# Optimization experiments

Measured on AMD Instinct MI355X. Metric: run time of the kernel, lower is better.

Reference implementation:

```python
import jax, jax.numpy as jnp
import numpy as np
from math import comb

DEGREE = 3


def build_index_tables(n, degree):
    """For each degree d in [2, degree], build (first, rest) int arrays so that
    row_d = x[first] * row_{d-1}[rest], where row_d lists the values of all
    ordered (multiset) degree-d monomials in lexicographic order.
    An ordered d-tuple starting with i has its tail t[1:] being an ordered
    (d-1)-tuple with elements in [i, n); in lexicographic order these occupy
    the tail of row_{d-1}, starting at prev_len - comb(n-i+d-2, d-1)."""
    tables = []
    prev_len = n  # row_1 = x itself
    for d in range(2, degree + 1):
        starts = np.array([prev_len - comb(n - i + d - 2, d - 1) for i in range(n)], dtype=np.int64)
        rest = np.concatenate([np.arange(s, prev_len, dtype=np.int32) for s in starts])
        first = np.repeat(np.arange(n, dtype=np.int32), prev_len - starts)
        tables.append((jnp.asarray(first), jnp.asarray(rest)))
        prev_len = rest.shape[0]
    return tables


def setup_inputs() -> dict:
    key = jax.random.key(0)
    n, out_size = 256, 32
    ks = jax.random.split(key, 5)
    sizes = [comb(n + d - 1, d) for d in range(DEGREE + 1)]  # [1, 256, 32896, 2829056]
    inp = {"x": jax.random.normal(ks[0], (n,), dtype=jnp.float32)}
    for d in range(DEGREE + 1):
        fan_in = sizes[d]
        bound = 1.0 / np.sqrt(fan_in)  # kaiming_uniform with a=sqrt(5)
        inp[f"coeff_deg_{d}"] = jax.random.uniform(
            ks[d + 1], (out_size, fan_in), dtype=jnp.float32, minval=-bound, maxval=bound)
    return inp


def reference(x, coeff_deg_0, coeff_deg_1, coeff_deg_2, coeff_deg_3):
    n = x.shape[0]
    tables = build_index_tables(n, DEGREE)  # static numpy work at trace time
    rows = [jnp.ones((1,), dtype=x.dtype), x]
    for first, rest in tables:
        rows.append(x[first] * rows[-1][rest])  # gather + elementwise product
    coeffs = [coeff_deg_0, coeff_deg_1, coeff_deg_2, coeff_deg_3]
    out = coeffs[0] @ rows[0]
    for c, r in zip(coeffs[1:], rows[1:]):
        out = out + c @ r  # (out_size, m_d) @ (m_d,) -> (out_size,)
    return out
```

## Files before the change

### kernel.cpp

```cpp
#include <hip/hip_runtime.h>

constexpr int N   = 256;
constexpr int OUT = 32;
constexpr int OPG = 8;
constexpr int OG  = OUT / OPG;
constexpr int M2  = 32896;
constexpr int M3  = 2829056;
constexpr int Q3  = M3 / 4;
constexpr int Q2  = M2 / 4;
constexpr int BX  = 256;
constexpr int IT3 = 11;
constexpr int D2_FIRST = 208;

typedef float f32x4 __attribute__((ext_vector_type(4)));

__device__ __forceinline__ int c3_tail(int s) {
    return s * (s + 1) * (s + 2) / 6;
}

__global__ __launch_bounds__(256, 4) void poly_partial(
    const float* __restrict__ x, const float* __restrict__ c2,
    const float* __restrict__ c3, float* __restrict__ partial)
{
    __shared__ float xs[N];
    const int tid = threadIdx.x;
    if (tid < N) xs[tid] = x[tid];
    __syncthreads();

    const int bx = blockIdx.x;
    const int g  = blockIdx.y;

    float acc[OPG];
#pragma unroll
    for (int oo = 0; oo < OPG; ++oo) acc[oo] = 0.f;

    const float* __restrict__ c3g = c3 + (size_t)g * OPG * M3;

    for (int it = 0; it < IT3; ++it) {
        const int q = bx * 256 + tid + it * (BX * 256);
        if (q < Q3) {
            const int base = q * 4;
            int lo = 0, hi = N - 1;
            while (lo < hi) {
                int mid = (lo + hi + 1) >> 1;
                int O = M3 - c3_tail(N - mid);
                if (O <= base) lo = mid; else hi = mid - 1;
            }
            const int i = lo;
            const int s = N - i;
            const int rem = base - (M3 - c3_tail(s));
            lo = 0; hi = s - 1;
            while (lo < hi) {
                int mid = (lo + hi + 1) >> 1;
                int A = mid * s - (mid * (mid - 1)) / 2;
                if (A <= rem) lo = mid; else hi = mid - 1;
            }
            const int a = lo;
            int ii = i, j = i + a, k = j + (rem - (a * s - (a * (a - 1)) / 2));

            float v[4];
#pragma unroll
            for (int t = 0; t < 4; ++t) {
                v[t] = xs[ii] * xs[j] * xs[k];
                ++k;
                if (k == N) { ++j; if (j == N) { ++ii; j = ii; } k = j; }
            }
            const float* p = c3g + base;
#pragma unroll
            for (int oo = 0; oo < OPG; ++oo) {
                const f32x4 c = __builtin_nontemporal_load(
                    reinterpret_cast<const f32x4*>(p + (size_t)oo * M3));
                acc[oo] += c[0] * v[0] + c[1] * v[1] + c[2] * v[2] + c[3] * v[3];
            }
        }
    }

    if (bx >= D2_FIRST) {
        const int q = (bx - D2_FIRST) * 256 + tid;
        if (q < Q2) {
            const int base = q * 4;
            int lo = 0, hi = N - 1;
            while (lo < hi) {
                int mid = (lo + hi + 1) >> 1;
                int O = mid * N - (mid * (mid - 1)) / 2;
                if (O <= base) lo = mid; else hi = mid - 1;
            }
            int j = lo;
            int k = j + (base - (j * N - (j * (j - 1)) / 2));
            float v[4];
#pragma unroll
            for (int t = 0; t < 4; ++t) {
                v[t] = xs[j] * xs[k];
                ++k;
                if (k == N) { ++j; k = j; }
            }
            const float* p = c2 + (size_t)g * OPG * M2 + base;
#pragma unroll
            for (int oo = 0; oo < OPG; ++oo) {
                const f32x4 c = __builtin_nontemporal_load(
                    reinterpret_cast<const f32x4*>(p + (size_t)oo * M2));
                acc[oo] += c[0] * v[0] + c[1] * v[1] + c[2] * v[2] + c[3] * v[3];
            }
        }
    }

    __shared__ float red[4][OPG];
    const int lane = tid & 63, wid = tid >> 6;
#pragma unroll
    for (int oo = 0; oo < OPG; ++oo) {
        float a = acc[oo];
#pragma unroll
        for (int off = 32; off > 0; off >>= 1) a += __shfl_down(a, off);
        if (lane == 0) red[wid][oo] = a;
    }
    __syncthreads();
    if (tid < OPG) {
        partial[((size_t)g * BX + bx) * OPG + tid] =
            red[0][tid] + red[1][tid] + red[2][tid] + red[3][tid];
    }
}

__global__ __launch_bounds__(1024) void poly_final(
    const float* __restrict__ partial, const float* __restrict__ x,
    const float* __restrict__ c0, const float* __restrict__ c1,
    float* __restrict__ out)
{
    __shared__ float lds[1024];
    const int tid = threadIdx.x;
    const int o = tid & 31, c = tid >> 5;
    const int g = o >> 3, oo = o & 7;

    float a = 0.f;
#pragma unroll
    for (int r = 0; r < BX / 32; ++r) {
        const int b = c + r * 32;
        a += partial[((size_t)g * BX + b) * OPG + oo];
    }
#pragma unroll
    for (int e = 0; e < 8; ++e) {
        const int k = c * 8 + e;
        a += c1[o * N + k] * x[k];
    }
    if (c == 0) a += c0[o];
    lds[tid] = a;
    __syncthreads();
    if (tid < 32) {
        float s = 0.f;
#pragma unroll
        for (int cc = 0; cc < 32; ++cc) s += lds[cc * 32 + tid];
        out[tid] = s;
    }
}

extern "C" void kernel_launch(void* const* d_in, const int* in_sizes, int n_in,
                              void* d_out, int out_size, void* d_ws, size_t ws_size,
                              hipStream_t stream) {
    const float* x  = (const float*)d_in[0];
    const float* c0 = (const float*)d_in[1];
    const float* c1 = (const float*)d_in[2];
    const float* c2 = (const float*)d_in[3];
    const float* c3 = (const float*)d_in[4];
    float* out     = (float*)d_out;
    float* partial = (float*)d_ws;

    dim3 grid(BX, OG);
    poly_partial<<<grid, 256, 0, stream>>>(x, c2, c3, partial);
    poly_final<<<1, 1024, 0, stream>>>(partial, x, c0, c1, out);
}
```

Measured before the change: 69.41 us.

## Process eight monomials per thread with contiguous per-block ranges and parallel final reduce

Each thread now handles 8 consecutive degree-3 (and degree-2) monomials, loading two float4 vectors per output row. The index binary searches are amortised over twice as many elements. Work is split into contiguous balanced chunks per block instead of a strided interleave, and degree-2 work is spread across all blocks. The final kernel runs 32 blocks that reduce with wave shuffles instead of a single 1024-thread block. Memory traffic per block becomes a contiguous range, which may change DRAM access locality; per-thread register use rises.

```diff
diff --git a/kernel.cpp b/kernel.cpp
--- a/kernel.cpp
+++ b/kernel.cpp
@@ -6,11 +6,14 @@
 constexpr int OG  = OUT / OPG;
 constexpr int M2  = 32896;
 constexpr int M3  = 2829056;
-constexpr int Q3  = M3 / 4;
-constexpr int Q2  = M2 / 4;
+constexpr int P3  = M3 / 8;
+constexpr int P2  = M2 / 8;
 constexpr int BX  = 256;
-constexpr int IT3 = 11;
-constexpr int D2_FIRST = 208;
+constexpr int K3  = P3 / BX;
+constexpr int R3  = P3 % BX;
+constexpr int K2  = P2 / BX;
+constexpr int R2  = P2 % BX;
+constexpr int IT3 = (K3 + 1 + 255) / 256;
 
 typedef float f32x4 __attribute__((ext_vector_type(4)));
 
@@ -34,51 +37,59 @@
 #pragma unroll
     for (int oo = 0; oo < OPG; ++oo) acc[oo] = 0.f;
 
-    const float* __restrict__ c3g = c3 + (size_t)g * OPG * M3;
+    {
+        const int s3 = bx * K3 + (bx < R3 ? bx : R3);
+        const int n3 = K3 + (bx < R3 ? 1 : 0);
+        const float* __restrict__ c3g = c3 + (size_t)g * OPG * M3;
+        for (int it = 0; it < IT3; ++it) {
+            const int r = it * 256 + tid;
+            if (r < n3) {
+                const int base = (s3 + r) * 8;
+                int lo = 0, hi = N - 1;
+                while (lo < hi) {
+                    int mid = (lo + hi + 1) >> 1;
+                    int O = M3 - c3_tail(N - mid);
+                    if (O <= base) lo = mid; else hi = mid - 1;
+                }
+                const int i = lo;
+                const int s = N - i;
+                const int rem = base - (M3 - c3_tail(s));
+                lo = 0; hi = s - 1;
+                while (lo < hi) {
+                    int mid = (lo + hi + 1) >> 1;
+                    int A = mid * s - (mid * (mid - 1)) / 2;
+                    if (A <= rem) lo = mid; else hi = mid - 1;
+                }
+                const int a = lo;
+                int ii = i, j = i + a, k = j + (rem - (a * s - (a * (a - 1)) / 2));
 
-    for (int it = 0; it < IT3; ++it) {
-        const int q = bx * 256 + tid + it * (BX * 256);
-        if (q < Q3) {
-            const int base = q * 4;
-            int lo = 0, hi = N - 1;
-            while (lo < hi) {
-                int mid = (lo + hi + 1) >> 1;
-                int O = M3 - c3_tail(N - mid);
-                if (O <= base) lo = mid; else hi = mid - 1;
-            }
-            const int i = lo;
-            const int s = N - i;
-            const int rem = base - (M3 - c3_tail(s));
-            lo = 0; hi = s - 1;
-            while (lo < hi) {
-                int mid = (lo + hi + 1) >> 1;
-                int A = mid * s - (mid * (mid - 1)) / 2;
-                if (A <= rem) lo = mid; else hi = mid - 1;
-            }
-            const int a = lo;
-            int ii = i, j = i + a, k = j + (rem - (a * s - (a * (a - 1)) / 2));
-
-            float v[4];
+                float v[8];
 #pragma unroll
-            for (int t = 0; t < 4; ++t) {
-                v[t] = xs[ii] * xs[j] * xs[k];
-                ++k;
-                if (k == N) { ++j; if (j == N) { ++ii; j = ii; } k = j; }
-            }
-            const float* p = c3g + base;
+                for (int t = 0; t < 8; ++t) {
+                    v[t] = xs[ii] * xs[j] * xs[k];
+                    ++k;
+                    if (k == N) { ++j; if (j == N) { ++ii; j = ii; } k = j; }
+                }
+                const float* p = c3g + (size_t)base;
 #pragma unroll
-            for (int oo = 0; oo < OPG; ++oo) {
-                const f32x4 c = __builtin_nontemporal_load(
-                    reinterpret_cast<const f32x4*>(p + (size_t)oo * M3));
-                acc[oo] += c[0] * v[0] + c[1] * v[1] + c[2] * v[2] + c[3] * v[3];
+                for (int oo = 0; oo < OPG; ++oo) {
+                    const float* sp = p + (size_t)oo * M3;
+                    const f32x4 ca = __builtin_nontemporal_load(
+                        reinterpret_cast<const f32x4*>(sp));
+                    const f32x4 cb = __builtin_nontemporal_load(
+                        reinterpret_cast<const f32x4*>(sp + 4));
+                    acc[oo] += ca[0] * v[0] + ca[1] * v[1] + ca[2] * v[2] + ca[3] * v[3]
+                             + cb[0] * v[4] + cb[1] * v[5] + cb[2] * v[6] + cb[3] * v[7];
+                }
             }
         }
     }
 
-    if (bx >= D2_FIRST) {
-        const int q = (bx - D2_FIRST) * 256 + tid;
-        if (q < Q2) {
-            const int base = q * 4;
+    {
+        const int s2 = bx * K2 + (bx < R2 ? bx : R2);
+        const int n2 = K2 + (bx < R2 ? 1 : 0);
+        if (tid < n2) {
+            const int base = (s2 + tid) * 8;
             int lo = 0, hi = N - 1;
             while (lo < hi) {
                 int mid = (lo + hi + 1) >> 1;
@@ -87,9 +98,9 @@
             }
             int j = lo;
             int k = j + (base - (j * N - (j * (j - 1)) / 2));
-            float v[4];
+            float v[8];
 #pragma unroll
-            for (int t = 0; t < 4; ++t) {
+            for (int t = 0; t < 8; ++t) {
                 v[t] = xs[j] * xs[k];
                 ++k;
                 if (k == N) { ++j; k = j; }
@@ -97,9 +108,13 @@
             const float* p = c2 + (size_t)g * OPG * M2 + base;
 #pragma unroll
             for (int oo = 0; oo < OPG; ++oo) {
-                const f32x4 c = __builtin_nontemporal_load(
-                    reinterpret_cast<const f32x4*>(p + (size_t)oo * M2));
-                acc[oo] += c[0] * v[0] + c[1] * v[1] + c[2] * v[2] + c[3] * v[3];
+                const float* sp = p + (size_t)oo * M2;
+                const f32x4 ca = __builtin_nontemporal_load(
+                    reinterpret_cast<const f32x4*>(sp));
+                const f32x4 cb = __builtin_nontemporal_load(
+                    reinterpret_cast<const f32x4*>(sp + 4));
+                acc[oo] += ca[0] * v[0] + ca[1] * v[1] + ca[2] * v[2] + ca[3] * v[3]
+                         + cb[0] * v[4] + cb[1] * v[5] + cb[2] * v[6] + cb[3] * v[7];
             }
         }
     }
@@ -120,36 +135,26 @@
     }
 }
 
-__global__ __launch_bounds__(1024) void poly_final(
+__global__ __launch_bounds__(256) void poly_final(
     const float* __restrict__ partial, const float* __restrict__ x,
     const float* __restrict__ c0, const float* __restrict__ c1,
     float* __restrict__ out)
 {
-    __shared__ float lds[1024];
+    const int o = blockIdx.x;
+    const int g = o >> 3, oo = o & 7;
     const int tid = threadIdx.x;
-    const int o = tid & 31, c = tid >> 5;
-    const int g = o >> 3, oo = o & 7;
 
-    float a = 0.f;
+    float a = partial[((size_t)g * BX + tid) * OPG + oo]
+            + c1[o * N + tid] * x[tid];
+
+    __shared__ float red[4];
+    const int lane = tid & 63, wid = tid >> 6;
 #pragma unroll
-    for (int r = 0; r < BX / 32; ++r) {
-        const int b = c + r * 32;
-        a += partial[((size_t)g * BX + b) * OPG + oo];
-    }
-#pragma unroll
-    for (int e = 0; e < 8; ++e) {
-        const int k = c * 8 + e;
-        a += c1[o * N + k] * x[k];
-    }
-    if (c == 0) a += c0[o];
-    lds[tid] = a;
+    for (int off = 32; off > 0; off >>= 1) a += __shfl_down(a, off);
+    if (lane == 0) red[wid] = a;
     __syncthreads();
-    if (tid < 32) {
-        float s = 0.f;
-#pragma unroll
-        for (int cc = 0; cc < 32; ++cc) s += lds[cc * 32 + tid];
-        out[tid] = s;
-    }
+    if (tid == 0)
+        out[o] = red[0] + red[1] + red[2] + red[3] + c0[o];
 }
 
 extern "C" void kernel_launch(void* const* d_in, const int* in_sizes, int n_in,
@@ -165,5 +170,5 @@
 
     dim3 grid(BX, OG);
     poly_partial<<<grid, 256, 0, stream>>>(x, c2, c3, partial);
-    poly_final<<<1, 1024, 0, stream>>>(partial, x, c0, c1, out);
+    poly_final<<<OUT, 256, 0, stream>>>(partial, x, c0, c1, out);
 }
```

After: 87.99 us. +26.8%, slower.

## Double-buffer degree-3 coefficient loads and parallelize final reduction across blocks

Applied to the files above, without the earlier changes.

The degree-3 loop is unrolled into templated steps that issue the next iteration's eight 16-byte coefficient loads into a second register buffer before computing the current monomials, so memory latency overlaps with the index binary searches. The monomial computation also hoists the x[i]*x[j] product. The final kernel now uses 32 blocks of 256 threads with wave shuffles instead of one 1024-thread block. The extra prefetch buffers raise register pressure, which could hurt occupancy under launch_bounds(256,4).

```diff
diff --git a/kernel.cpp b/kernel.cpp
--- a/kernel.cpp
+++ b/kernel.cpp
@@ -18,6 +18,61 @@
     return s * (s + 1) * (s + 2) / 6;
 }
 
+template<int IT>
+__device__ __forceinline__ void step3(const float* __restrict__ c3g,
+                                      const float* xs, int q0,
+                                      f32x4 (&cons)[OPG], f32x4 (&pref)[OPG],
+                                      float (&acc)[OPG])
+{
+    if constexpr (IT + 1 < IT3) {
+        const int qn = q0 + (IT + 1) * (BX * 256);
+        if (qn < Q3) {
+            const float* pn = c3g + (size_t)qn * 4;
+#pragma unroll
+            for (int oo = 0; oo < OPG; ++oo)
+                pref[oo] = __builtin_nontemporal_load(
+                    reinterpret_cast<const f32x4*>(pn + (size_t)oo * M3));
+        }
+    }
+    const int q = q0 + IT * (BX * 256);
+    if (q < Q3) {
+        const int base = q * 4;
+        int lo = 0, hi = N - 1;
+        while (lo < hi) {
+            int mid = (lo + hi + 1) >> 1;
+            int O = M3 - c3_tail(N - mid);
+            if (O <= base) lo = mid; else hi = mid - 1;
+        }
+        const int i0 = lo;
+        const int s = N - i0;
+        const int rem = base - (M3 - c3_tail(s));
+        lo = 0; hi = s - 1;
+        while (lo < hi) {
+            int mid = (lo + hi + 1) >> 1;
+            int A = mid * s - (mid * (mid - 1)) / 2;
+            if (A <= rem) lo = mid; else hi = mid - 1;
+        }
+        const int a = lo;
+        int ii = i0, j = i0 + a, k = j + (rem - (a * s - (a * (a - 1)) / 2));
+
+        float pre = xs[ii] * xs[j];
+        float v[4];
+#pragma unroll
+        for (int t = 0; t < 4; ++t) {
+            v[t] = pre * xs[k];
+            ++k;
+            if (k == N) {
+                ++j; if (j == N) { ++ii; j = ii; }
+                k = j; pre = xs[ii] * xs[j];
+            }
+        }
+#pragma unroll
+        for (int oo = 0; oo < OPG; ++oo)
+            acc[oo] += cons[oo][0] * v[0] + cons[oo][1] * v[1]
+                     + cons[oo][2] * v[2] + cons[oo][3] * v[3];
+    }
+}
+
 __global__ __launch_bounds__(256, 4) void poly_partial(
     const float* __restrict__ x, const float* __restrict__ c2,
     const float* __restrict__ c3, float* __restrict__ partial)
@@ -31,54 +86,40 @@
     const int g  = blockIdx.y;
 
     float acc[OPG];
-#pragma unroll
-    for (int oo = 0; oo < OPG; ++oo) acc[oo] = 0.f;
+    f32x4 bufA[OPG], bufB[OPG];
+#pragma unroll
+    for (int oo = 0; oo < OPG; ++oo) {
+        acc[oo] = 0.f;
+        bufA[oo] = f32x4{0.f, 0.f, 0.f, 0.f};
+        bufB[oo] = f32x4{0.f, 0.f, 0.f, 0.f};
+    }
 
     const float* __restrict__ c3g = c3 + (size_t)g * OPG * M3;
-
-    for (int it = 0; it < IT3; ++it) {
-        const int q = bx * 256 + tid + it * (BX * 256);
-        if (q < Q3) {
-            const int base = q * 4;
-            int lo = 0, hi = N - 1;
-            while (lo < hi) {
-                int mid = (lo + hi + 1) >> 1;
-                int O = M3 - c3_tail(N - mid);
-                if (O <= base) lo = mid; else hi = mid - 1;
-            }
-            const int i = lo;
-            const int s = N - i;
-            const int rem = base - (M3 - c3_tail(s));
-            lo = 0; hi = s - 1;
-            while (lo < hi) {
-                int mid = (lo + hi + 1) >> 1;
-                int A = mid * s - (mid * (mid - 1)) / 2;
-                if (A <= rem) lo = mid; else hi = mid - 1;
-            }
-            const int a = lo;
-            int ii = i, j = i + a, k = j + (rem - (a * s - (a * (a - 1)) / 2));
-
-            float v[4];
-#pragma unroll
-            for (int t = 0; t < 4; ++t) {
-                v[t] = xs[ii] * xs[j] * xs[k];
-                ++k;
-                if (k == N) { ++j; if (j == N) { ++ii; j = ii; } k = j; }
-            }
-            const float* p = c3g + base;
-#pragma unroll
-            for (int oo = 0; oo < OPG; ++oo) {
-                const f32x4 c = __builtin_nontemporal_load(
-                    reinterpret_cast<const f32x4*>(p + (size_t)oo * M3));
-                acc[oo] += c[0] * v[0] + c[1] * v[1] + c[2] * v[2] + c[3] * v[3];
-            }
-        }
-    }
+    const int q0 = bx * 256 + tid;
+
+    {
+        const float* p0 = c3g + (size_t)q0 * 4;
+#pragma unroll
+        for (int oo = 0; oo < OPG; ++oo)
+            bufA[oo] = __builtin_nontemporal_load(
+                reinterpret_cast<const f32x4*>(p0 + (size_t)oo * M3));
+    }
+    step3<0>(c3g, xs, q0, bufA, bufB, acc);
+    step3<1>(c3g, xs, q0, bufB, bufA, acc);
+    step3<2>(c3g, xs, q0, bufA, bufB, acc);
+    step3<3>(c3g, xs, q0, bufB, bufA, acc);
+    step3<4>(c3g, xs, q0, bufA, bufB, acc);
+    step3<5>(c3g, xs, q0, bufB, bufA, acc);
+    step3<6>(c3g, xs, q0, bufA, bufB, acc);
+    step3<7>(c3g, xs, q0, bufB, bufA, acc);
+    step3<8>(c3g, xs, q0, bufA, bufB, acc);
+    step3<9>(c3g, xs, q0, bufB, bufA, acc);
+    step3<10>(c3g, xs, q0, bufA, bufB, acc);
 
     if (bx >= D2_FIRST) {
-        const int q = (bx - D2_FIRST) * 256 + tid;
-        if (q < Q2) {
-            const int base = q * 4;
+        const int qq = (bx - D2_FIRST) * 256 + tid;
+        if (qq < Q2) {
+            const int base = qq * 4;
             int lo = 0, hi = N - 1;
             while (lo < hi) {
                 int mid = (lo + hi + 1) >> 1;
@@ -87,12 +128,13 @@
             }
             int j = lo;
             int k = j + (base - (j * N - (j * (j - 1)) / 2));
+            float pre = xs[j];
             float v[4];
 #pragma unroll
             for (int t = 0; t < 4; ++t) {
-                v[t] = xs[j] * xs[k];
+                v[t] = pre * xs[k];
                 ++k;
-                if (k == N) { ++j; k = j; }
+                if (k == N) { ++j; k = j; pre = xs[j]; }
             }
             const float* p = c2 + (size_t)g * OPG * M2 + base;
 #pragma unroll
@@ -120,36 +162,26 @@
     }
 }
 
-__global__ __launch_bounds__(1024) void poly_final(
+__global__ __launch_bounds__(256) void poly_final(
     const float* __restrict__ partial, const float* __restrict__ x,
     const float* __restrict__ c0, const float* __restrict__ c1,
     float* __restrict__ out)
 {
-    __shared__ float lds[1024];
+    const int o = blockIdx.x;
+    const int g = o >> 3, oo = o & 7;
     const int tid = threadIdx.x;
-    const int o = tid & 31, c = tid >> 5;
-    const int g = o >> 3, oo = o & 7;
-
-    float a = 0.f;
-#pragma unroll
-    for (int r = 0; r < BX / 32; ++r) {
-        const int b = c + r * 32;
-        a += partial[((size_t)g * BX + b) * OPG + oo];
-    }
-#pragma unroll
-    for (int e = 0; e < 8; ++e) {
-        const int k = c * 8 + e;
-        a += c1[o * N + k] * x[k];
-    }
-    if (c == 0) a += c0[o];
-    lds[tid] = a;
+
+    float a = partial[((size_t)g * BX + tid) * OPG + oo]
+            + c1[o * N + tid] * x[tid];
+
+    __shared__ float red[4];
+    const int lane = tid & 63, wid = tid >> 6;
+#pragma unroll
+    for (int off = 32; off > 0; off >>= 1) a += __shfl_down(a, off);
+    if (lane == 0) red[wid] = a;
     __syncthreads();
-    if (tid < 32) {
-        float s = 0.f;
-#pragma unroll
-        for (int cc = 0; cc < 32; ++cc) s += lds[cc * 32 + tid];
-        out[tid] = s;
-    }
+    if (tid == 0)
+        out[o] = red[0] + red[1] + red[2] + red[3] + c0[o];
 }
 
 extern "C" void kernel_launch(void* const* d_in, const int* in_sizes, int n_in,
@@ -165,5 +197,5 @@
 
     dim3 grid(BX, OG);
     poly_partial<<<grid, 256, 0, stream>>>(x, c2, c3, partial);
-    poly_final<<<1, 1024, 0, stream>>>(partial, x, c0, c1, out);
-}
+    poly_final<<<OUT, 256, 0, stream>>>(partial, x, c0, c1, out);
+}
```

Measured after the change: 66.90 us. 1.04x faster.
